# Optimization experiments

Hardware: AMD Instinct MI355X
Metric: run time of the kernel (lower is better)

Reference implementation:

```python
import jax, jax.numpy as jnp
import numpy as np

N = 256        # number of nodes (= len(num_nodes_phases))
F = 16         # max_features = max(num_nodes_phases)
H = 2048       # hidden_dim
P = 16         # phases per node (uniform -> all q heads output P)
E = 32768      # directed edges


def setup_inputs() -> dict:
    key = jax.random.key(0)
    k1, k2, k3, k4 = jax.random.split(key, 4)
    x_list = jax.random.normal(k1, (N, F), dtype=jnp.float32)
    edge_index = jax.random.randint(k2, (2, E), 0, N, dtype=jnp.int64)
    # GCNConv weight/bias (PyG: x @ W then aggregate, bias added after)
    W = jax.random.normal(k3, (F, H), dtype=jnp.float32) * (1.0 / np.sqrt(F))
    b = jnp.zeros((H,), dtype=jnp.float32)
    # per-node q-value heads, stacked: Wq[n] is the n-th nn.Linear(H, P)
    Wq = jax.random.normal(k4, (N, H, P), dtype=jnp.float32) * (1.0 / np.sqrt(H))
    bq = jnp.zeros((N, P), dtype=jnp.float32)
    return {"x_list": x_list, "edge_index": edge_index, "W": W, "b": b, "Wq": Wq, "bq": bq}


def reference(x_list, edge_index, W, b, Wq, bq):
    n = x_list.shape[0]
    # GCNConv: add self-loops, symmetric degree normalization
    loops = jnp.arange(n, dtype=edge_index.dtype)
    src = jnp.concatenate([edge_index[0], loops])
    dst = jnp.concatenate([edge_index[1], loops])
    deg = jax.ops.segment_sum(jnp.ones_like(dst, dtype=x_list.dtype), dst, num_segments=n)
    dinv = jnp.where(deg > 0, jax.lax.rsqrt(deg), 0.0).astype(x_list.dtype)
    norm = dinv[src] * dinv[dst]                      # [E+N]
    h = x_list @ W                                    # [N, H]
    msg = h[src] * norm[:, None]                      # [E+N, H] (dominant traffic)
    out = jax.ops.segment_sum(msg, dst, num_segments=n) + b  # [N, H]
    # per-node-type linear heads (batched over nodes)
    q = jnp.einsum('nh,nhp->np', out, Wq) + bq        # [N, P]
    return q
```

## Files before the change

kernel.cpp:

```cpp
#include <hip/hip_runtime.h>

#define N_NODES 256
#define F_DIM   16
#define H_DIM   2048
#define P_DIM   16
#define E_EDGES 32768
#define BLK     512


__global__ __launch_bounds__(256) void k_cnt(const int* __restrict__ ei,
                                             float* __restrict__ cnt,
                                             float* __restrict__ deg) {
    int e = blockIdx.x * 256 + threadIdx.x;
    int s = ei[e];
    int d = ei[E_EDGES + e];
    atomicAdd(&cnt[d * N_NODES + s], 1.0f);
    atomicAdd(&deg[d], 1.0f);
}

__global__ __launch_bounds__(BLK) void k_node(
    const float* __restrict__ cnt, const float* __restrict__ deg,
    const float* __restrict__ x,   const float* __restrict__ W,
    const float* __restrict__ b,   const float* __restrict__ Wq,
    const float* __restrict__ bq,  float* __restrict__ qout)
{
    __shared__ float gw[4][F_DIM];
    __shared__ float gfin[F_DIM];
    __shared__ float red[BLK / 64][P_DIM];

    const int n = blockIdx.x;
    const int t = threadIdx.x;
    const int w = t >> 6, l = t & 63;

    const float4* Wqn = (const float4*)(Wq + (size_t)n * (H_DIM * P_DIM));
    float4 u00, u01, u02, u03, u10, u11, u12, u13;
    float4 u20, u21, u22, u23, u30, u31, u32, u33;
    {
        int h0 = (t          ) * 4;
        int h1 = (t +     BLK) * 4;
        int h2 = (t + 2 * BLK) * 4;
        int h3 = (t + 3 * BLK) * 4;
        u00 = Wqn[h0 + 0]; u01 = Wqn[h0 + 1]; u02 = Wqn[h0 + 2]; u03 = Wqn[h0 + 3];
        u10 = Wqn[h1 + 0]; u11 = Wqn[h1 + 1]; u12 = Wqn[h1 + 2]; u13 = Wqn[h1 + 3];
        u20 = Wqn[h2 + 0]; u21 = Wqn[h2 + 1]; u22 = Wqn[h2 + 2]; u23 = Wqn[h2 + 3];
        u30 = Wqn[h3 + 0]; u31 = Wqn[h3 + 1]; u32 = Wqn[h3 + 2]; u33 = Wqn[h3 + 3];
    }

    float dn = rsqrtf(deg[n] + 1.0f);

    if (t < N_NODES) {
        float dt = rsqrtf(deg[t] + 1.0f);
        float a  = (cnt[n * N_NODES + t] + (t == n ? 1.0f : 0.0f)) * dt;
        const float4* x4 = (const float4*)(x + t * F_DIM);
        float4 a0 = x4[0], a1 = x4[1], a2 = x4[2], a3 = x4[3];
        float val[F_DIM];
        val[0]  = a * a0.x; val[1]  = a * a0.y; val[2]  = a * a0.z; val[3]  = a * a0.w;
        val[4]  = a * a1.x; val[5]  = a * a1.y; val[6]  = a * a1.z; val[7]  = a * a1.w;
        val[8]  = a * a2.x; val[9]  = a * a2.y; val[10] = a * a2.z; val[11] = a * a2.w;
        val[12] = a * a3.x; val[13] = a * a3.y; val[14] = a * a3.z; val[15] = a * a3.w;
#pragma unroll
        for (int f = 0; f < F_DIM; ++f)
#pragma unroll
            for (int off = 32; off > 0; off >>= 1)
                val[f] += __shfl_xor(val[f], off, 64);
        if (l == 0) {
#pragma unroll
            for (int f = 0; f < F_DIM; ++f) gw[w][f] = val[f];
        }
    }
    __syncthreads();
    if (t < F_DIM)
        gfin[t] = gw[0][t] + gw[1][t] + gw[2][t] + gw[3][t];
    __syncthreads();

    float gr[F_DIM];
#pragma unroll
    for (int f = 0; f < F_DIM; ++f) gr[f] = gfin[f] * dn;

    float o[4];
#pragma unroll
    for (int i = 0; i < 4; ++i) {
        int hh = t + BLK * i;
        float v = b[hh];
#pragma unroll
        for (int f = 0; f < F_DIM; ++f)
            v += gr[f] * W[f * H_DIM + hh];
        o[i] = v;
    }

    float acc[16];
#pragma unroll
    for (int p = 0; p < 16; ++p) acc[p] = 0.0f;

#define ACC4(OV, U0, U1, U2, U3) { float ov = (OV);                            \
    acc[0]  += ov * U0.x; acc[1]  += ov * U0.y; acc[2]  += ov * U0.z; acc[3]  += ov * U0.w; \
    acc[4]  += ov * U1.x; acc[5]  += ov * U1.y; acc[6]  += ov * U1.z; acc[7]  += ov * U1.w; \
    acc[8]  += ov * U2.x; acc[9]  += ov * U2.y; acc[10] += ov * U2.z; acc[11] += ov * U2.w; \
    acc[12] += ov * U3.x; acc[13] += ov * U3.y; acc[14] += ov * U3.z; acc[15] += ov * U3.w; }

    ACC4(o[0], u00, u01, u02, u03)
    ACC4(o[1], u10, u11, u12, u13)
    ACC4(o[2], u20, u21, u22, u23)
    ACC4(o[3], u30, u31, u32, u33)
#undef ACC4

#pragma unroll
    for (int p = 0; p < 16; ++p)
#pragma unroll
        for (int off = 32; off > 0; off >>= 1)
            acc[p] += __shfl_down(acc[p], off, 64);

    if (l == 0) {
#pragma unroll
        for (int p = 0; p < 16; ++p) red[w][p] = acc[p];
    }
    __syncthreads();
    if (t < P_DIM) {
        float s = bq[n * P_DIM + t];
#pragma unroll
        for (int ww = 0; ww < BLK / 64; ++ww) s += red[ww][t];
        qout[n * P_DIM + t] = s;
    }
}

extern "C" void kernel_launch(void* const* d_in, const int* in_sizes, int n_in,
                              void* d_out, int out_size, void* d_ws, size_t ws_size,
                              hipStream_t stream) {
    const float* x  = (const float*)d_in[0];
    const int*   ei = (const int*)d_in[1];
    const float* W  = (const float*)d_in[2];
    const float* b  = (const float*)d_in[3];
    const float* Wq = (const float*)d_in[4];
    const float* bq = (const float*)d_in[5];
    float* qout = (float*)d_out;

    float* cnt = (float*)d_ws;
    float* deg = cnt + N_NODES * N_NODES;

    hipMemsetAsync(d_ws, 0, (N_NODES * N_NODES + N_NODES) * sizeof(float), stream);
    k_cnt <<<E_EDGES / 256, 256, 0, stream>>>(ei, cnt, deg);
    k_node<<<N_NODES, BLK, 0, stream>>>(cnt, deg, x, W, b, Wq, bq, qout);
}
```

Measured before the change: 110.0 us.

## Fuse edge counting into node kernel with per-block shared-memory histograms

Drops the memset and the separate global-atomic counting kernel. Each block now scans all edges itself, builds a per-wave degree histogram in LDS, and counts only the edges whose destination is its own node. Each block re-reads the whole edge list (256 KB per block), but this removes two launches, the global atomics and the round-trip through the dense count matrix. The Wq loads are interleaved with the edge scan so their latency overlaps the histogram work.

```diff
diff --git a/kernel.cpp b/kernel.cpp
--- a/kernel.cpp
+++ b/kernel.cpp
@@ -6,51 +6,59 @@
 #define P_DIM   16
 #define E_EDGES 32768
 #define BLK     512
+#define NW      (BLK / 64)
 
-
-__global__ __launch_bounds__(256) void k_cnt(const int* __restrict__ ei,
-                                             float* __restrict__ cnt,
-                                             float* __restrict__ deg) {
-    int e = blockIdx.x * 256 + threadIdx.x;
-    int s = ei[e];
-    int d = ei[E_EDGES + e];
-    atomicAdd(&cnt[d * N_NODES + s], 1.0f);
-    atomicAdd(&deg[d], 1.0f);
-}
-
-__global__ __launch_bounds__(BLK) void k_node(
-    const float* __restrict__ cnt, const float* __restrict__ deg,
-    const float* __restrict__ x,   const float* __restrict__ W,
-    const float* __restrict__ b,   const float* __restrict__ Wq,
-    const float* __restrict__ bq,  float* __restrict__ qout)
+__global__ __launch_bounds__(BLK) void k_fused(
+    const int* __restrict__ ei,   const float* __restrict__ x,
+    const float* __restrict__ W,  const float* __restrict__ b,
+    const float* __restrict__ Wq, const float* __restrict__ bq,
+    float* __restrict__ qout)
 {
-    __shared__ float gw[4][F_DIM];
-    __shared__ float gfin[F_DIM];
-    __shared__ float red[BLK / 64][P_DIM];
+    __shared__ unsigned histw[NW][N_NODES];
+    __shared__ unsigned cntrow[N_NODES];
+    __shared__ float    dinv[N_NODES];
+    __shared__ float    gw[4][F_DIM];
+    __shared__ float    gfin[F_DIM];
+    __shared__ float    red[NW][P_DIM];
 
     const int n = blockIdx.x;
     const int t = threadIdx.x;
     const int w = t >> 6, l = t & 63;
 
+#pragma unroll
+    for (int i = 0; i < 4; ++i) ((unsigned*)histw)[t + i * BLK] = 0u;
+    if (t < N_NODES) cntrow[t] = 0u;
+    __syncthreads();
+
     const float4* Wqn = (const float4*)(Wq + (size_t)n * (H_DIM * P_DIM));
-    float4 u00, u01, u02, u03, u10, u11, u12, u13;
-    float4 u20, u21, u22, u23, u30, u31, u32, u33;
-    {
-        int h0 = (t          ) * 4;
-        int h1 = (t +     BLK) * 4;
-        int h2 = (t + 2 * BLK) * 4;
-        int h3 = (t + 3 * BLK) * 4;
-        u00 = Wqn[h0 + 0]; u01 = Wqn[h0 + 1]; u02 = Wqn[h0 + 2]; u03 = Wqn[h0 + 3];
-        u10 = Wqn[h1 + 0]; u11 = Wqn[h1 + 1]; u12 = Wqn[h1 + 2]; u13 = Wqn[h1 + 3];
-        u20 = Wqn[h2 + 0]; u21 = Wqn[h2 + 1]; u22 = Wqn[h2 + 2]; u23 = Wqn[h2 + 3];
-        u30 = Wqn[h3 + 0]; u31 = Wqn[h3 + 1]; u32 = Wqn[h3 + 2]; u33 = Wqn[h3 + 3];
+    float4 u[16];
+#pragma unroll
+    for (int k = 0; k < 16; ++k) {
+        const int base = (k << 11) + (t << 2);
+        int4 s4 = *(const int4*)(ei + base);
+        int4 d4 = *(const int4*)(ei + E_EDGES + base);
+        u[k] = Wqn[(t + ((k >> 2) * BLK)) * 4 + (k & 3)];
+        atomicAdd(&histw[w][d4.x], 1u);
+        atomicAdd(&histw[w][d4.y], 1u);
+        atomicAdd(&histw[w][d4.z], 1u);
+        atomicAdd(&histw[w][d4.w], 1u);
+        if (d4.x == n) atomicAdd(&cntrow[s4.x], 1u);
+        if (d4.y == n) atomicAdd(&cntrow[s4.y], 1u);
+        if (d4.z == n) atomicAdd(&cntrow[s4.z], 1u);
+        if (d4.w == n) atomicAdd(&cntrow[s4.w], 1u);
     }
-
-    float dn = rsqrtf(deg[n] + 1.0f);
+    __syncthreads();
 
     if (t < N_NODES) {
-        float dt = rsqrtf(deg[t] + 1.0f);
-        float a  = (cnt[n * N_NODES + t] + (t == n ? 1.0f : 0.0f)) * dt;
+        unsigned dg = 0;
+#pragma unroll
+        for (int i = 0; i < NW; ++i) dg += histw[i][t];
+        dinv[t] = rsqrtf((float)dg + 1.0f);
+    }
+    __syncthreads();
+
+    if (t < N_NODES) {
+        float a = ((float)cntrow[t] + (t == n ? 1.0f : 0.0f)) * dinv[t];
         const float4* x4 = (const float4*)(x + t * F_DIM);
         float4 a0 = x4[0], a1 = x4[1], a2 = x4[2], a3 = x4[3];
         float val[F_DIM];
@@ -73,6 +81,7 @@
         gfin[t] = gw[0][t] + gw[1][t] + gw[2][t] + gw[3][t];
     __syncthreads();
 
+    const float dn = dinv[n];
     float gr[F_DIM];
 #pragma unroll
     for (int f = 0; f < F_DIM; ++f) gr[f] = gfin[f] * dn;
@@ -98,10 +107,10 @@
     acc[8]  += ov * U2.x; acc[9]  += ov * U2.y; acc[10] += ov * U2.z; acc[11] += ov * U2.w; \
     acc[12] += ov * U3.x; acc[13] += ov * U3.y; acc[14] += ov * U3.z; acc[15] += ov * U3.w; }
 
-    ACC4(o[0], u00, u01, u02, u03)
-    ACC4(o[1], u10, u11, u12, u13)
-    ACC4(o[2], u20, u21, u22, u23)
-    ACC4(o[3], u30, u31, u32, u33)
+    ACC4(o[0], u[0],  u[1],  u[2],  u[3])
+    ACC4(o[1], u[4],  u[5],  u[6],  u[7])
+    ACC4(o[2], u[8],  u[9],  u[10], u[11])
+    ACC4(o[3], u[12], u[13], u[14], u[15])
 #undef ACC4
 
 #pragma unroll
@@ -118,7 +127,7 @@
     if (t < P_DIM) {
         float s = bq[n * P_DIM + t];
 #pragma unroll
-        for (int ww = 0; ww < BLK / 64; ++ww) s += red[ww][t];
+        for (int ww = 0; ww < NW; ++ww) s += red[ww][t];
         qout[n * P_DIM + t] = s;
     }
 }
@@ -134,10 +143,6 @@
     const float* bq = (const float*)d_in[5];
     float* qout = (float*)d_out;
 
-    float* cnt = (float*)d_ws;
-    float* deg = cnt + N_NODES * N_NODES;
-
-    hipMemsetAsync(d_ws, 0, (N_NODES * N_NODES + N_NODES) * sizeof(float), stream);
-    k_cnt <<<E_EDGES / 256, 256, 0, stream>>>(ei, cnt, deg);
-    k_node<<<N_NODES, BLK, 0, stream>>>(cnt, deg, x, W, b, Wq, bq, qout);
+    (void)d_ws; (void)ws_size;
+    k_fused<<<N_NODES, BLK, 0, stream>>>(ei, x, W, b, Wq, bq, qout);
 }
```

New measurement: 95.63 us. -13.1%, faster.
